# Kernel optimization log

Measured on AMD Instinct MI355X. Metric: run time of the kernel, lower is better.

Reference implementation:

```python
import jax, jax.numpy as jnp
import numpy as np

N, D, HEADS = 8192, 1024, 8
SCALE = float(np.sqrt(D / HEADS))  # sqrt(dim_head) = sqrt(128)


def setup_inputs() -> dict:
    key = jax.random.key(0)
    ks = jax.random.split(key, 9)
    std = 0.02
    return {
        "x": jax.random.normal(ks[0], (N, D), dtype=jnp.float32),
        "Wq": jax.random.normal(ks[1], (D, D), dtype=jnp.float32) * std,
        "bq": jax.random.normal(ks[2], (D,), dtype=jnp.float32) * std,
        "Wk": jax.random.normal(ks[3], (D, D), dtype=jnp.float32) * std,
        "bk": jax.random.normal(ks[4], (D,), dtype=jnp.float32) * std,
        "Wv": jax.random.normal(ks[5], (D, D), dtype=jnp.float32) * std,
        "bv": jax.random.normal(ks[6], (D,), dtype=jnp.float32) * std,
        "Wo": jax.random.normal(ks[7], (D, D), dtype=jnp.float32) * std,
        "bo": jax.random.normal(ks[8], (D,), dtype=jnp.float32) * std,
    }


def reference(x, Wq, bq, Wk, bk, Wv, bv, Wo, bo):
    # torch nn.Linear: y = x @ W.T + b
    q = x @ Wq.T + bq          # [N, D]
    k = x @ Wk.T + bk          # [N, D]
    v = x @ Wv.T + bv          # [N, D]
    z = q @ k.T                # [N, N]
    att = jax.nn.softmax(z / SCALE, axis=-1)  # softmax over keys (torch dim=1 for 2D)
    out = att @ v              # [N, D]
    out = out @ Wo.T + bo      # output projection
    return out + x             # residual
```

## Files before the change

### kernel.cpp

```cpp
#include <hip/hip_runtime.h>
#include <stdint.h>


#define NTOK 8192
#define DMOD 1024
static constexpr float INV_SCALE = 0.08838834764831845f;

typedef __attribute__((ext_vector_type(8))) short short8;
typedef __attribute__((ext_vector_type(4))) float f32x4;
typedef __attribute__((ext_vector_type(4))) unsigned short u16x4;

__device__ __forceinline__ unsigned short f2bf(float f) {
  union { float f; uint32_t u; } x{f};
  uint32_t r = x.u + 0x7fffu + ((x.u >> 16) & 1u);
  return (unsigned short)(r >> 16);
}
__device__ __forceinline__ void async16(void* lds, const void* g) {
  __builtin_amdgcn_global_load_lds((const __attribute__((address_space(1))) void*)g,
                                   (__attribute__((address_space(3))) void*)lds, 16, 0, 0);
}
__device__ __forceinline__ f32x4 mfma16(short8 a, short8 b, f32x4 c) {
  return __builtin_amdgcn_mfma_f32_16x16x32_bf16(a, b, c, 0, 0, 0);
}
template<int N> __device__ __forceinline__ void waitvm() {
  if constexpr (N == 0)       asm volatile("s_waitcnt vmcnt(0)" ::: "memory");
  else if constexpr (N == 3)  asm volatile("s_waitcnt vmcnt(3)" ::: "memory");
  else if constexpr (N == 4)  asm volatile("s_waitcnt vmcnt(4)" ::: "memory");
  else if constexpr (N == 6)  asm volatile("s_waitcnt vmcnt(6)" ::: "memory");
  else if constexpr (N == 8)  asm volatile("s_waitcnt vmcnt(8)" ::: "memory");
  else if constexpr (N == 9)  asm volatile("s_waitcnt vmcnt(9)" ::: "memory");
  else if constexpr (N == 12) asm volatile("s_waitcnt vmcnt(12)" ::: "memory");
  else static_assert(N == 0, "unsupported vmcnt");
}

__global__ __launch_bounds__(256) void cast_f32_bf16(const float* __restrict__ in,
                                                     unsigned short* __restrict__ out, int n4) {
  int i = blockIdx.x * 256 + threadIdx.x;
  int stride = gridDim.x * 256;
  for (; i < n4; i += stride) {
    float4 v = ((const float4*)in)[i];
    u16x4 o;
    o[0] = f2bf(v.x); o[1] = f2bf(v.y); o[2] = f2bf(v.z); o[3] = f2bf(v.w);
    ((u16x4*)out)[i] = o;
  }
}

template<int BM, int BN, int WM, int WN, bool BIAS, bool TRANS, bool F32OUT, bool RES, bool EXPO, bool ONES>
__global__ __launch_bounds__(WM*WN*64, 2) void gemm_pipe(
    const unsigned short* __restrict__ A, const unsigned short* __restrict__ B,
    unsigned short* __restrict__ O16, float* __restrict__ O32,
    const float* __restrict__ bias, const float* __restrict__ resid,
    int M, int N, int K, float scale)
{
  constexpr int THREADS = WM * WN * 64;
  constexpr int M_REP = BM / (WM * 16);
  constexpr int N_REP = BN / (WN * 16);
  constexpr int ABYTES = BM * 64;
  constexpr int BBYTES = BN * 64;
  constexpr int BUFB = ABYTES + BBYTES;
  constexpr int LOADS = BUFB / (THREADS * 16);
  static_assert(BUFB % (THREADS * 16) == 0, "staging must tile the buffer");
  static_assert(ABYTES % (THREADS * 16) == 0, "A region aligns to load boundary");

  __shared__ alignas(16) char lds[4 * BUFB];

  const int t = threadIdx.x;
  const int l = t & 63, w = t >> 6;
  const int wrow = (w / WN) * (M_REP * 16);
  const int wcol = (w % WN) * (N_REP * 16);

  const int nwg = gridDim.x * gridDim.y;
  const int flat = blockIdx.y * gridDim.x + blockIdx.x;
  const int q8 = nwg >> 3, r8 = nwg & 7;
  const int xcd = flat & 7, pos = flat >> 3;
  const int swz = (xcd < r8 ? xcd * (q8 + 1) : r8 * (q8 + 1) + (xcd - r8) * q8) + pos;
  const int row0 = (swz / gridDim.x) * BM;
  const int col0 = (swz % gridDim.x) * BN;

  const unsigned short* gsrc[LOADS];
  int ldst[LOADS];
#pragma unroll
  for (int li = 0; li < LOADS; ++li) {
    const int byte0 = li * THREADS * 16 + t * 16;
    int r; const unsigned short* base;
    if (byte0 < ABYTES) { r = byte0 >> 6; base = A + (size_t)(row0 + r) * K; }
    else { r = (byte0 - ABYTES) >> 6; base = B + (size_t)(col0 + r) * K; }
    const int slot = (byte0 >> 4) & 3;
    gsrc[li] = base + (slot ^ ((r >> 1) & 3)) * 8;
    ldst[li] = byte0;
  }

  int offA[M_REP], offB[N_REP];
#pragma unroll
  for (int m = 0; m < M_REP; ++m) {
    int r = wrow + m * 16 + (l & 15);
    offA[m] = r * 64 + (((l >> 4) ^ ((r >> 1) & 3)) * 16);
  }
#pragma unroll
  for (int n = 0; n < N_REP; ++n) {
    int r = wcol + n * 16 + (l & 15);
    offB[n] = ABYTES + r * 64 + (((l >> 4) ^ ((r >> 1) & 3)) * 16);
  }

  short8 bones;
#pragma unroll
  for (int i = 0; i < 8; ++i) bones[i] = (short)0x3F80;

  f32x4 acc[M_REP][N_REP] = {};
  f32x4 accrs[M_REP] = {};
  const int KT = K / 32;

#pragma unroll
  for (int j = 0; j < 3; ++j) {
    char* bb = lds + j * BUFB;
#pragma unroll
    for (int s = 0; s < LOADS; ++s) async16(bb + ldst[s], gsrc[s] + j * 32);
  }

  for (int t3 = 0; t3 < KT; ++t3) {
    asm volatile("s_waitcnt lgkmcnt(0)" ::: "memory");
    __builtin_amdgcn_s_barrier();
    asm volatile("" ::: "memory");
    if (t3 + 3 < KT) {
      char* bb = lds + ((t3 + 3) & 3) * BUFB;
#pragma unroll
      for (int s = 0; s < LOADS; ++s) async16(bb + ldst[s], gsrc[s] + (size_t)(t3 + 3) * 32);
      waitvm<3 * LOADS>();
    } else if (t3 + 3 == KT) {
      waitvm<2 * LOADS>();
    } else if (t3 + 2 == KT) {
      waitvm<LOADS>();
    } else {
      waitvm<0>();
    }
    __builtin_amdgcn_s_barrier();
    asm volatile("" ::: "memory");

    const char* bb = lds + (t3 & 3) * BUFB;
    short8 af[M_REP], bf[N_REP];
#pragma unroll
    for (int m = 0; m < M_REP; ++m) af[m] = *(const short8*)(bb + offA[m]);
#pragma unroll
    for (int n = 0; n < N_REP; ++n) bf[n] = *(const short8*)(bb + offB[n]);
#pragma unroll
    for (int m = 0; m < M_REP; ++m)
#pragma unroll
      for (int n = 0; n < N_REP; ++n)
        acc[m][n] = mfma16(af[m], bf[n], acc[m][n]);
    if constexpr (ONES) {
#pragma unroll
      for (int m = 0; m < M_REP; ++m) accrs[m] = mfma16(af[m], bones, accrs[m]);
    }
  }

  const int rr = (l >> 4) * 4;
  if constexpr (EXPO) {
#pragma unroll
    for (int m = 0; m < M_REP; ++m)
#pragma unroll
      for (int n = 0; n < N_REP; ++n)
#pragma unroll
        for (int j = 0; j < 4; ++j) {
          const int r = row0 + wrow + m * 16 + rr + j;
          const int c = col0 + wcol + n * 16 + (l & 15);
          O16[(size_t)r * N + c] = f2bf(__expf(acc[m][n][j] - 3.0f));
        }
  } else if constexpr (ONES) {
#pragma unroll
    for (int m = 0; m < M_REP; ++m)
#pragma unroll
      for (int j = 0; j < 4; ++j) {
        const float inv = 1.0f / accrs[m][j];
        const int r = row0 + wrow + m * 16 + rr + j;
#pragma unroll
        for (int n = 0; n < N_REP; ++n) {
          const int c = col0 + wcol + n * 16 + (l & 15);
          O16[(size_t)r * N + c] = f2bf(acc[m][n][j] * inv);
        }
      }
  } else {
#pragma unroll
    for (int m = 0; m < M_REP; ++m)
#pragma unroll
      for (int n = 0; n < N_REP; ++n)
#pragma unroll
        for (int j = 0; j < 4; ++j) {
          int r = row0 + wrow + m * 16 + rr + j;
          int c = col0 + wcol + n * 16 + (l & 15);
          float v = acc[m][n][j];
          if (BIAS) v += bias[c];
          v *= scale;
          if (RES) v += resid[(size_t)r * N + c];
          if (F32OUT) O32[(size_t)r * N + c] = v;
          else if (TRANS) O16[(size_t)c * M + r] = f2bf(v);
          else O16[(size_t)r * N + c] = f2bf(v);
        }
  }
}

extern "C" void kernel_launch(void* const* d_in, const int* in_sizes, int n_in,
                              void* d_out, int out_size, void* d_ws, size_t ws_size,
                              hipStream_t stream) {
  const float* x  = (const float*)d_in[0];
  const float* Wq = (const float*)d_in[1];
  const float* bq = (const float*)d_in[2];
  const float* Wk = (const float*)d_in[3];
  const float* bk = (const float*)d_in[4];
  const float* Wv = (const float*)d_in[5];
  const float* bv = (const float*)d_in[6];
  const float* Wo = (const float*)d_in[7];
  const float* bo = (const float*)d_in[8];
  float* out = (float*)d_out;

  char* p = (char*)d_ws;
  unsigned short* xb  = (unsigned short*)p; p += (size_t)NTOK * DMOD * 2;
  unsigned short* Wqb = (unsigned short*)p; p += (size_t)DMOD * DMOD * 2;
  unsigned short* Wkb = (unsigned short*)p; p += (size_t)DMOD * DMOD * 2;
  unsigned short* Wvb = (unsigned short*)p; p += (size_t)DMOD * DMOD * 2;
  unsigned short* Wob = (unsigned short*)p; p += (size_t)DMOD * DMOD * 2;
  unsigned short* Qb  = (unsigned short*)p; p += (size_t)NTOK * DMOD * 2;
  unsigned short* Kb  = (unsigned short*)p; p += (size_t)NTOK * DMOD * 2;
  unsigned short* Vt  = (unsigned short*)p; p += (size_t)DMOD * NTOK * 2;
  unsigned short* Ob  = (unsigned short*)p; p += (size_t)NTOK * DMOD * 2;
  unsigned short* S   = (unsigned short*)p; p += (size_t)NTOK * NTOK * 2;

  cast_f32_bf16<<<dim3(2048), dim3(256), 0, stream>>>(x, xb, NTOK * DMOD / 4);
  cast_f32_bf16<<<dim3(1024), dim3(256), 0, stream>>>(Wq, Wqb, DMOD * DMOD / 4);
  cast_f32_bf16<<<dim3(1024), dim3(256), 0, stream>>>(Wk, Wkb, DMOD * DMOD / 4);
  cast_f32_bf16<<<dim3(1024), dim3(256), 0, stream>>>(Wv, Wvb, DMOD * DMOD / 4);
  cast_f32_bf16<<<dim3(1024), dim3(256), 0, stream>>>(Wo, Wob, DMOD * DMOD / 4);

  dim3 b512(512), b256(256);
  dim3 gS(NTOK / 256, NTOK / 256);
  dim3 gProj(DMOD / 128, NTOK / 128);
  dim3 gPV(DMOD / 256, NTOK / 128);

  gemm_pipe<128,128,2,2,true,false,false,false,false,false><<<gProj, b256, 0, stream>>>(xb, Wqb, Qb, nullptr, bq, nullptr, NTOK, DMOD, DMOD, INV_SCALE);
  gemm_pipe<128,128,2,2,true,false,false,false,false,false><<<gProj, b256, 0, stream>>>(xb, Wkb, Kb, nullptr, bk, nullptr, NTOK, DMOD, DMOD, 1.0f);
  gemm_pipe<128,128,2,2,true,true,false,false,false,false><<<gProj, b256, 0, stream>>>(xb, Wvb, Vt, nullptr, bv, nullptr, NTOK, DMOD, DMOD, 1.0f);
  gemm_pipe<256,256,2,4,false,false,false,false,true,false><<<gS, b512, 0, stream>>>(Qb, Kb, S, nullptr, nullptr, nullptr, NTOK, NTOK, DMOD, 1.0f);
  gemm_pipe<128,256,2,4,false,false,false,false,false,true><<<gPV, b512, 0, stream>>>(S, Vt, Ob, nullptr, nullptr, nullptr, NTOK, DMOD, NTOK, 1.0f);
  gemm_pipe<128,128,2,2,true,false,true,true,false,false><<<gProj, b256, 0, stream>>>(Ob, Wob, nullptr, out, bo, x, NTOK, DMOD, DMOD, 1.0f);
}
```

Before: 516.3 us.

## Add 8-wave ping-pong GEMM kernel for QK^T and PV with interleaved loads

```diff
diff --git a/kernel.cpp b/kernel.cpp
--- a/kernel.cpp
+++ b/kernel.cpp
@@ -45,7 +45,231 @@
   }
 }
 
-template<int BM, int BN, int WM, int WN, bool BIAS, bool TRANS, bool F32OUT, bool RES, bool EXPO, bool ONES>
+template<int BM, int BN, bool EXPO, bool ONES>
+__global__ __launch_bounds__(512, 2) void gemm_8p(
+    const unsigned short* __restrict__ A, const unsigned short* __restrict__ B,
+    unsigned short* __restrict__ O16, int M, int N, int K)
+{
+  constexpr int M_REP = BM / 32;
+  constexpr int N_REP = BN / 64;
+  constexpr int M2 = M_REP / 2, N2 = N_REP / 2;
+  constexpr int ABY = BM * 128;
+  constexpr int BBY = BN * 128;
+  constexpr int BUFB = ABY + BBY;
+  constexpr int HLA = (ABY / 2) / 8192;
+  constexpr int HLB = (BBY / 2) / 8192;
+  constexpr int TL = 2 * (HLA + HLB);
+  static_assert((ABY / 2) % 8192 == 0 && (BBY / 2) % 8192 == 0);
+
+  __shared__ alignas(16) char lds[2 * BUFB];
+
+  const int t = threadIdx.x;
+  const int l = t & 63, w = t >> 6;
+  const int g = w >> 2, h = w & 3;
+
+  const int nwg = gridDim.x * gridDim.y;
+  const int flat = blockIdx.y * gridDim.x + blockIdx.x;
+  const int q8 = nwg >> 3, r8 = nwg & 7;
+  const int xcd = flat & 7, pos = flat >> 3;
+  const int swz = (xcd < r8 ? xcd * (q8 + 1) : r8 * (q8 + 1) + (xcd - r8) * q8) + pos;
+  const int row0 = (swz / gridDim.x) * BM;
+  const int col0 = (swz % gridDim.x) * BN;
+
+  const unsigned short* gAlo[HLA]; int dAlo[HLA];
+  const unsigned short* gAhi[HLA]; int dAhi[HLA];
+  const unsigned short* gBlo[HLB]; int dBlo[HLB];
+  const unsigned short* gBhi[HLB]; int dBhi[HLB];
+#pragma unroll
+  for (int i = 0; i < HLA; ++i) {
+    const int rel = i * 8192 + t * 16;
+    const int slot = (rel >> 4) & 7;
+    { int row = rel >> 7;
+      gAlo[i] = A + (size_t)(row0 + row) * K + ((slot ^ (row & 7)) * 8);
+      dAlo[i] = rel; }
+    { int row = (rel >> 7) + BM / 2;
+      gAhi[i] = A + (size_t)(row0 + row) * K + ((slot ^ (row & 7)) * 8);
+      dAhi[i] = ABY / 2 + rel; }
+  }
+#pragma unroll
+  for (int i = 0; i < HLB; ++i) {
+    const int rel = i * 8192 + t * 16;
+    const int slot = (rel >> 4) & 7;
+    { int row = rel >> 7;
+      gBlo[i] = B + (size_t)(col0 + row) * K + ((slot ^ (row & 7)) * 8);
+      dBlo[i] = ABY + rel; }
+    { int row = (rel >> 7) + BN / 2;
+      gBhi[i] = B + (size_t)(col0 + row) * K + ((slot ^ (row & 7)) * 8);
+      dBhi[i] = ABY + BBY / 2 + rel; }
+  }
+
+  int offA[M_REP][2], offB[N_REP][2];
+#pragma unroll
+  for (int m = 0; m < M_REP; ++m) {
+    const int r = (m * 2 + g) * 16 + (l & 15);
+#pragma unroll
+    for (int k = 0; k < 2; ++k)
+      offA[m][k] = r * 128 + (((k * 4 + (l >> 4)) ^ (r & 7)) * 16);
+  }
+#pragma unroll
+  for (int n = 0; n < N_REP; ++n) {
+    const int r = (n * 4 + h) * 16 + (l & 15);
+#pragma unroll
+    for (int k = 0; k < 2; ++k)
+      offB[n][k] = ABY + r * 128 + (((k * 4 + (l >> 4)) ^ (r & 7)) * 16);
+  }
+
+  short8 bones;
+#pragma unroll
+  for (int i = 0; i < 8; ++i) bones[i] = (short)0x3F80;
+
+  f32x4 acc[M_REP][N_REP] = {};
+  f32x4 accrs[M_REP] = {};
+  const int KT = K / 64;
+
+#pragma unroll
+  for (int j = 0; j < 2; ++j) {
+    char* bb = lds + j * BUFB;
+#pragma unroll
+    for (int i = 0; i < HLA; ++i) async16(bb + dAlo[i], gAlo[i] + j * 64);
+#pragma unroll
+    for (int i = 0; i < HLB; ++i) async16(bb + dBlo[i], gBlo[i] + j * 64);
+#pragma unroll
+    for (int i = 0; i < HLB; ++i) async16(bb + dBhi[i], gBhi[i] + j * 64);
+#pragma unroll
+    for (int i = 0; i < HLA; ++i) async16(bb + dAhi[i], gAhi[i] + j * 64);
+  }
+  waitvm<TL>();
+  __builtin_amdgcn_s_barrier();
+
+  for (int T = 0; T < KT; ++T) {
+    const char* rb = lds + (T & 1) * BUFB;
+    char* sb = lds + (T & 1) * BUFB;
+    const bool st = (T + 2) < KT;
+    const size_t ko = (size_t)(T + 2) * 64;
+    short8 fAlo[M2][2], fAhi[M2][2], fBlo[N2][2], fBhi[N2][2];
+
+#pragma unroll
+    for (int m = 0; m < M2; ++m) { fAlo[m][0] = *(const short8*)(rb + offA[m][0]);
+                                   fAlo[m][1] = *(const short8*)(rb + offA[m][1]); }
+#pragma unroll
+    for (int n = 0; n < N2; ++n) { fBlo[n][0] = *(const short8*)(rb + offB[n][0]);
+                                   fBlo[n][1] = *(const short8*)(rb + offB[n][1]); }
+    __builtin_amdgcn_s_barrier();
+    asm volatile("s_waitcnt lgkmcnt(0)" ::: "memory");
+    __builtin_amdgcn_s_setprio(1);
+#pragma unroll
+    for (int m = 0; m < M2; ++m)
+#pragma unroll
+      for (int n = 0; n < N2; ++n) {
+        acc[m][n] = mfma16(fAlo[m][0], fBlo[n][0], acc[m][n]);
+        acc[m][n] = mfma16(fAlo[m][1], fBlo[n][1], acc[m][n]);
+      }
+    if constexpr (ONES) {
+#pragma unroll
+      for (int m = 0; m < M2; ++m) {
+        accrs[m] = mfma16(fAlo[m][0], bones, accrs[m]);
+        accrs[m] = mfma16(fAlo[m][1], bones, accrs[m]);
+      }
+    }
+    __builtin_amdgcn_s_setprio(0);
+    __builtin_amdgcn_s_barrier();
+
+#pragma unroll
+    for (int n = 0; n < N2; ++n) { fBhi[n][0] = *(const short8*)(rb + offB[N2 + n][0]);
+                                   fBhi[n][1] = *(const short8*)(rb + offB[N2 + n][1]); }
+    if (st) {
+#pragma unroll
+      for (int i = 0; i < HLA; ++i) async16(sb + dAlo[i], gAlo[i] + ko);
+    }
+    __builtin_amdgcn_s_barrier();
+    asm volatile("s_waitcnt lgkmcnt(0)" ::: "memory");
+    __builtin_amdgcn_s_setprio(1);
+#pragma unroll
+    for (int m = 0; m < M2; ++m)
+#pragma unroll
+      for (int n = 0; n < N2; ++n) {
+        acc[m][N2 + n] = mfma16(fAlo[m][0], fBhi[n][0], acc[m][N2 + n]);
+        acc[m][N2 + n] = mfma16(fAlo[m][1], fBhi[n][1], acc[m][N2 + n]);
+      }
+    __builtin_amdgcn_s_setprio(0);
+    __builtin_amdgcn_s_barrier();
+
+#pragma unroll
+    for (int m = 0; m < M2; ++m) { fAhi[m][0] = *(const short8*)(rb + offA[M2 + m][0]);
+                                   fAhi[m][1] = *(const short8*)(rb + offA[M2 + m][1]); }
+    if (st) {
+#pragma unroll
+      for (int i = 0; i < HLB; ++i) async16(sb + dBlo[i], gBlo[i] + ko);
+    }
+    __builtin_amdgcn_s_barrier();
+    asm volatile("s_waitcnt lgkmcnt(0)" ::: "memory");
+    __builtin_amdgcn_s_setprio(1);
+#pragma unroll
+    for (int m = 0; m < M2; ++m)
+#pragma unroll
+      for (int n = 0; n < N2; ++n) {
+        acc[M2 + m][N2 + n] = mfma16(fAhi[m][0], fBhi[n][0], acc[M2 + m][N2 + n]);
+        acc[M2 + m][N2 + n] = mfma16(fAhi[m][1], fBhi[n][1], acc[M2 + m][N2 + n]);
+      }
+    if constexpr (ONES) {
+#pragma unroll
+      for (int m = 0; m < M2; ++m) {
+        accrs[M2 + m] = mfma16(fAhi[m][0], bones, accrs[M2 + m]);
+        accrs[M2 + m] = mfma16(fAhi[m][1], bones, accrs[M2 + m]);
+      }
+    }
+    __builtin_amdgcn_s_setprio(0);
+    __builtin_amdgcn_s_barrier();
+
+    if (st) {
+#pragma unroll
+      for (int i = 0; i < HLB; ++i) async16(sb + dBhi[i], gBhi[i] + ko);
+#pragma unroll
+      for (int i = 0; i < HLA; ++i) async16(sb + dAhi[i], gAhi[i] + ko);
+    }
+    __builtin_amdgcn_s_setprio(1);
+#pragma unroll
+    for (int m = 0; m < M2; ++m)
+#pragma unroll
+      for (int n = 0; n < N2; ++n) {
+        acc[M2 + m][n] = mfma16(fAhi[m][0], fBlo[n][0], acc[M2 + m][n]);
+        acc[M2 + m][n] = mfma16(fAhi[m][1], fBlo[n][1], acc[M2 + m][n]);
+      }
+    __builtin_amdgcn_s_setprio(0);
+    if (st) waitvm<TL>();
+    else if (T + 1 < KT) waitvm<0>();
+    __builtin_amdgcn_s_barrier();
+  }
+
+  const int rr = (l >> 4) * 4;
+  if constexpr (EXPO) {
+#pragma unroll
+    for (int m = 0; m < M_REP; ++m)
+#pragma unroll
+      for (int n = 0; n < N_REP; ++n)
+#pragma unroll
+        for (int j = 0; j < 4; ++j) {
+          const int r = row0 + (m * 2 + g) * 16 + rr + j;
+          const int c = col0 + (n * 4 + h) * 16 + (l & 15);
+          O16[(size_t)r * N + c] = f2bf(__expf(acc[m][n][j] - 3.0f));
+        }
+  } else {
+#pragma unroll
+    for (int m = 0; m < M_REP; ++m)
+#pragma unroll
+      for (int j = 0; j < 4; ++j) {
+        const float inv = 1.0f / accrs[m][j];
+        const int r = row0 + (m * 2 + g) * 16 + rr + j;
+#pragma unroll
+        for (int n = 0; n < N_REP; ++n) {
+          const int c = col0 + (n * 4 + h) * 16 + (l & 15);
+          O16[(size_t)r * N + c] = f2bf(acc[m][n][j] * inv);
+        }
+      }
+  }
+}
+
+template<int BM, int BN, int WM, int WN, bool BIAS, bool TRANS, bool F32OUT, bool RES>
 __global__ __launch_bounds__(WM*WN*64, 2) void gemm_pipe(
     const unsigned short* __restrict__ A, const unsigned short* __restrict__ B,
     unsigned short* __restrict__ O16, float* __restrict__ O32,
@@ -59,8 +283,8 @@
   constexpr int BBYTES = BN * 64;
   constexpr int BUFB = ABYTES + BBYTES;
   constexpr int LOADS = BUFB / (THREADS * 16);
-  static_assert(BUFB % (THREADS * 16) == 0, "staging must tile the buffer");
-  static_assert(ABYTES % (THREADS * 16) == 0, "A region aligns to load boundary");
+  static_assert(BUFB % (THREADS * 16) == 0);
+  static_assert(ABYTES % (THREADS * 16) == 0);
 
   __shared__ alignas(16) char lds[4 * BUFB];
 
@@ -102,12 +326,7 @@
     offB[n] = ABYTES + r * 64 + (((l >> 4) ^ ((r >> 1) & 3)) * 16);
   }
 
-  short8 bones;
-#pragma unroll
-  for (int i = 0; i < 8; ++i) bones[i] = (short)0x3F80;
-
   f32x4 acc[M_REP][N_REP] = {};
-  f32x4 accrs[M_REP] = {};
   const int KT = K / 32;
 
 #pragma unroll
@@ -147,55 +366,25 @@
 #pragma unroll
       for (int n = 0; n < N_REP; ++n)
         acc[m][n] = mfma16(af[m], bf[n], acc[m][n]);
-    if constexpr (ONES) {
-#pragma unroll
-      for (int m = 0; m < M_REP; ++m) accrs[m] = mfma16(af[m], bones, accrs[m]);
-    }
   }
 
   const int rr = (l >> 4) * 4;
-  if constexpr (EXPO) {
-#pragma unroll
-    for (int m = 0; m < M_REP; ++m)
-#pragma unroll
-      for (int n = 0; n < N_REP; ++n)
-#pragma unroll
-        for (int j = 0; j < 4; ++j) {
-          const int r = row0 + wrow + m * 16 + rr + j;
-          const int c = col0 + wcol + n * 16 + (l & 15);
-          O16[(size_t)r * N + c] = f2bf(__expf(acc[m][n][j] - 3.0f));
-        }
-  } else if constexpr (ONES) {
-#pragma unroll
-    for (int m = 0; m < M_REP; ++m)
+#pragma unroll
+  for (int m = 0; m < M_REP; ++m)
+#pragma unroll
+    for (int n = 0; n < N_REP; ++n)
 #pragma unroll
       for (int j = 0; j < 4; ++j) {
-        const float inv = 1.0f / accrs[m][j];
-        const int r = row0 + wrow + m * 16 + rr + j;
-#pragma unroll
-        for (int n = 0; n < N_REP; ++n) {
-          const int c = col0 + wcol + n * 16 + (l & 15);
-          O16[(size_t)r * N + c] = f2bf(acc[m][n][j] * inv);
-        }
-      }
-  } else {
-#pragma unroll
-    for (int m = 0; m < M_REP; ++m)
-#pragma unroll
-      for (int n = 0; n < N_REP; ++n)
-#pragma unroll
-        for (int j = 0; j < 4; ++j) {
-          int r = row0 + wrow + m * 16 + rr + j;
-          int c = col0 + wcol + n * 16 + (l & 15);
-          float v = acc[m][n][j];
-          if (BIAS) v += bias[c];
-          v *= scale;
-          if (RES) v += resid[(size_t)r * N + c];
-          if (F32OUT) O32[(size_t)r * N + c] = v;
-          else if (TRANS) O16[(size_t)c * M + r] = f2bf(v);
-          else O16[(size_t)r * N + c] = f2bf(v);
-        }
-  }
+        int r = row0 + wrow + m * 16 + rr + j;
+        int c = col0 + wcol + n * 16 + (l & 15);
+        float v = acc[m][n][j];
+        if (BIAS) v += bias[c];
+        v *= scale;
+        if (RES) v += resid[(size_t)r * N + c];
+        if (F32OUT) O32[(size_t)r * N + c] = v;
+        else if (TRANS) O16[(size_t)c * M + r] = f2bf(v);
+        else O16[(size_t)r * N + c] = f2bf(v);
+      }
 }
 
 extern "C" void kernel_launch(void* const* d_in, const int* in_sizes, int n_in,
@@ -235,10 +424,10 @@
   dim3 gProj(DMOD / 128, NTOK / 128);
   dim3 gPV(DMOD / 256, NTOK / 128);
 
-  gemm_pipe<128,128,2,2,true,false,false,false,false,false><<<gProj, b256, 0, stream>>>(xb, Wqb, Qb, nullptr, bq, nullptr, NTOK, DMOD, DMOD, INV_SCALE);
-  gemm_pipe<128,128,2,2,true,false,false,false,false,false><<<gProj, b256, 0, stream>>>(xb, Wkb, Kb, nullptr, bk, nullptr, NTOK, DMOD, DMOD, 1.0f);
-  gemm_pipe<128,128,2,2,true,true,false,false,false,false><<<gProj, b256, 0, stream>>>(xb, Wvb, Vt, nullptr, bv, nullptr, NTOK, DMOD, DMOD, 1.0f);
-  gemm_pipe<256,256,2,4,false,false,false,false,true,false><<<gS, b512, 0, stream>>>(Qb, Kb, S, nullptr, nullptr, nullptr, NTOK, NTOK, DMOD, 1.0f);
-  gemm_pipe<128,256,2,4,false,false,false,false,false,true><<<gPV, b512, 0, stream>>>(S, Vt, Ob, nullptr, nullptr, nullptr, NTOK, DMOD, NTOK, 1.0f);
-  gemm_pipe<128,128,2,2,true,false,true,true,false,false><<<gProj, b256, 0, stream>>>(Ob, Wob, nullptr, out, bo, x, NTOK, DMOD, DMOD, 1.0f);
-}
+  gemm_pipe<128,128,2,2,true,false,false,false><<<gProj, b256, 0, stream>>>(xb, Wqb, Qb, nullptr, bq, nullptr, NTOK, DMOD, DMOD, INV_SCALE);
+  gemm_pipe<128,128,2,2,true,false,false,false><<<gProj, b256, 0, stream>>>(xb, Wkb, Kb, nullptr, bk, nullptr, NTOK, DMOD, DMOD, 1.0f);
+  gemm_pipe<128,128,2,2,true,true,false,false><<<gProj, b256, 0, stream>>>(xb, Wvb, Vt, nullptr, bv, nullptr, NTOK, DMOD, DMOD, 1.0f);
+  gemm_8p<256,256,true,false><<<gS, b512, 0, stream>>>(Qb, Kb, S, NTOK, NTOK, DMOD);
+  gemm_8p<128,256,false,true><<<gPV, b512, 0, stream>>>(S, Vt, Ob, NTOK, DMOD, NTOK);
+  gemm_pipe<128,128,2,2,true,false,true,true><<<gProj, b256, 0, stream>>>(Ob, Wob, nullptr, out, bo, x, NTOK, DMOD, DMOD, 1.0f);
+}
```

After: 512.6 us. About the same (-0.7%).
